# Optimization experiments

Hardware: AMD Instinct MI355X
Metric: run time of the kernel (lower is better)

Reference implementation:

```python
import jax, jax.numpy as jnp
import numpy as np

ALPHA = 0.4
STEPS = 4
EPSILON = 0.005

N_NODES = 4096
N_EDGES = 131072
D_FEAT = 128


def setup_inputs() -> dict:
    key = jax.random.key(0)
    k1, k2, k3, k4 = jax.random.split(key, 4)
    x = jax.random.normal(k1, (N_NODES, D_FEAT), dtype=jnp.float32)
    src = jax.random.randint(k2, (N_EDGES,), 0, N_NODES)
    dst = jax.random.randint(k3, (N_EDGES,), 0, N_NODES)
    edge_index = jnp.stack([src, dst], axis=0).astype(jnp.int64)
    edge_attr = jax.random.uniform(k4, (N_EDGES,), dtype=jnp.float32)
    return {"x": x, "edge_index": edge_index, "edge_attr": edge_attr}


def reference(x, edge_index, edge_attr):
    # PPR power series: result = sum_i theta_i * A_i, where
    #   A_0 = edge pattern with unit values, A_1 = A (edge_attr),
    #   A_{i+1} = threshold_eps(A @ A_i).
    # Dense [N,N] representation: thresholding (dropping entries < eps in the
    # sparse original) is exactly zeroing those entries here; jit-compatible
    # since sparse nnz is data-dependent.
    N = x.shape[0]
    src, dst = edge_index[0], edge_index[1]
    A = jnp.zeros((N, N), dtype=edge_attr.dtype).at[src, dst].add(edge_attr)
    P0 = jnp.zeros((N, N), dtype=edge_attr.dtype).at[src, dst].add(1.0)

    mats = [P0, A]
    for _ in range(1, STEPS - 1):
        M = A @ mats[-1]
        M = jnp.where(M >= EPSILON, M, jnp.zeros((), dtype=M.dtype))
        mats.append(M)

    thetas = [ALPHA * (1.0 - ALPHA) ** i for i in range(STEPS)]
    out = thetas[0] * mats[0]
    for t, m in zip(thetas[1:], mats[1:]):
        out = out + t * m
    return out
```

## Files before the change

kernel.cpp:

```cpp
#include <hip/hip_runtime.h>
#include <hip/hip_fp16.h>

#define N_NODES 4096
#define EPS 0.005f
#define TH0 0.4f
#define TH1 0.24f
#define TH2 0.144f
#define TH3 0.0864f
#define JTILE 512
#define NTILES (N_NODES / JTILE)
#define RCAP 80
#define CPAD 16

typedef float v4f __attribute__((ext_vector_type(4)));
typedef unsigned int u32x4 __attribute__((ext_vector_type(4)));


static __device__ __forceinline__ unsigned short f2h(float f) {
    return __half_as_ushort(__float2half(f));
}

__global__ void scatter_kernel(const int* __restrict__ idx,
                               const float* __restrict__ attr, int E,
                               int* __restrict__ counts, int2* __restrict__ pairs) {
    int e = blockIdx.x * blockDim.x + threadIdx.x;
    if (e < E) {
        int s = idx[e];
        int d = idx[e + E];
        float a = attr[e];
        int pos = atomicAdd(&counts[s * CPAD], 1);
        if (pos < RCAP) pairs[s * RCAP + pos] = make_int2(d, __float_as_int(a));
    }
}

__global__ __launch_bounds__(256)
void m2_kernel(const int* __restrict__ counts, const int2* __restrict__ pairs,
               unsigned short* __restrict__ m2) {
    __shared__ float acc[N_NODES];
    __shared__ int   kcol[RCAP];
    __shared__ float kval[RCAP];
    __shared__ int   kcnt[RCAP];
    int i = blockIdx.x;
    int t = threadIdx.x;
    float4 z = make_float4(0.f, 0.f, 0.f, 0.f);
    for (int j4 = t; j4 < N_NODES / 4; j4 += 256) ((float4*)acc)[j4] = z;
    int cnt = min(counts[i * CPAD], RCAP);
    if (t < cnt) {
        int2 p = pairs[i * RCAP + t];
        kcol[t] = p.x;
        kval[t] = __int_as_float(p.y);
        kcnt[t] = min(counts[p.x * CPAD], RCAP);
    }
    __syncthreads();
    int gid = t >> 3, gl = t & 7;
    int2 zp = make_int2(0, 0);
    for (int q = gid; q < cnt; q += 32) {
        float a = kval[q];
        int fb = kcol[q] * RCAP;
        int fn = kcnt[q];
        for (int f0 = gl; f0 < fn; f0 += 32) {
            int i1 = f0 + 8, i2 = f0 + 16, i3 = f0 + 24;
            int2 p0 = pairs[fb + f0];
            int2 p1 = (i1 < fn) ? pairs[fb + i1] : zp;
            int2 p2 = (i2 < fn) ? pairs[fb + i2] : zp;
            int2 p3 = (i3 < fn) ? pairs[fb + i3] : zp;
            unsafeAtomicAdd(&acc[p0.x], a * __int_as_float(p0.y));
            unsafeAtomicAdd(&acc[p1.x], a * __int_as_float(p1.y));
            unsafeAtomicAdd(&acc[p2.x], a * __int_as_float(p2.y));
            unsafeAtomicAdd(&acc[p3.x], a * __int_as_float(p3.y));
        }
    }
    __syncthreads();
    size_t rb = (size_t)i * N_NODES;
    for (int j4 = t; j4 < N_NODES / 4; j4 += 256) {
        float4 v = ((const float4*)acc)[j4];
        ushort4 r;
        r.x = (v.x >= EPS) ? f2h(v.x) : (unsigned short)0;
        r.y = (v.y >= EPS) ? f2h(v.y) : (unsigned short)0;
        r.z = (v.z >= EPS) ? f2h(v.z) : (unsigned short)0;
        r.w = (v.w >= EPS) ? f2h(v.w) : (unsigned short)0;
        ((ushort4*)(m2 + rb))[j4] = r;
    }
}

#define MIX2(uu_word, aclo, achi, aa)                                          \
    asm("v_fma_mix_f32 %0, %1, %2, %0 op_sel_hi:[0,1,0]"                       \
        : "+v"(aclo) : "v"(aa), "v"(uu_word));                                 \
    asm("v_fma_mix_f32 %0, %1, %2, %0 op_sel:[0,1,0] op_sel_hi:[0,1,0]"        \
        : "+v"(achi) : "v"(aa), "v"(uu_word));

#define MIX8(uu, aa)                                                           \
    MIX2(uu.x, ac0, ac1, aa) MIX2(uu.y, ac2, ac3, aa)                          \
    MIX2(uu.z, ac4, ac5, aa) MIX2(uu.w, ac6, ac7, aa)

__global__ __launch_bounds__(128)
void out_kernel(const int* __restrict__ counts, const int2* __restrict__ pairs,
                const unsigned short* __restrict__ m2,
                float* __restrict__ out) {
    __shared__ float ap[2][JTILE];
    int lin = blockIdx.x;
    int tile = lin & 7;
    int jb = tile * JTILE;
    int t = threadIdx.x;
    int w = t >> 6, lane = t & 63;
    int i = 2 * (lin >> 3) + w;
    float* apw = ap[w];
    ((float4*)apw)[lane] = make_float4(0.f, 0.f, 0.f, 0.f);
    ((float4*)apw)[64 + lane] = make_float4(0.f, 0.f, 0.f, 0.f);
    int cnt = min(counts[i * CPAD], RCAP);
    const int2* pi = pairs + i * RCAP;
    for (int e = lane; e < cnt; e += 64) {
        int2 p = pi[e];
        int cl = p.x - jb;
        if ((unsigned)cl < (unsigned)JTILE)
            unsafeAtomicAdd(&apw[cl], TH0 + TH1 * __int_as_float(p.y));
    }
    int cnt8 = (cnt + 7) & ~7;
    const unsigned short* m2l = m2 + jb + 8 * lane;
    float ac0 = 0.f, ac1 = 0.f, ac2 = 0.f, ac3 = 0.f;
    float ac4 = 0.f, ac5 = 0.f, ac6 = 0.f, ac7 = 0.f;
    for (int e = 0; e < cnt8; e += 8) {
        int4 q01 = *(const int4*)(pi + e);
        int4 q23 = *(const int4*)(pi + e + 2);
        int4 q45 = *(const int4*)(pi + e + 4);
        int4 q67 = *(const int4*)(pi + e + 6);
        int k0 = __builtin_amdgcn_readfirstlane(q01.x);
        int k1 = __builtin_amdgcn_readfirstlane(q01.z);
        int k2 = __builtin_amdgcn_readfirstlane(q23.x);
        int k3 = __builtin_amdgcn_readfirstlane(q23.z);
        int k4 = __builtin_amdgcn_readfirstlane(q45.x);
        int k5 = __builtin_amdgcn_readfirstlane(q45.z);
        int k6 = __builtin_amdgcn_readfirstlane(q67.x);
        int k7 = __builtin_amdgcn_readfirstlane(q67.z);
        float a0 = __int_as_float(q01.y), a1 = __int_as_float(q01.w);
        float a2 = __int_as_float(q23.y), a3 = __int_as_float(q23.w);
        float a4 = __int_as_float(q45.y), a5 = __int_as_float(q45.w);
        float a6 = __int_as_float(q67.y), a7 = __int_as_float(q67.w);
        u32x4 u0 = *(const u32x4*)(m2l + (size_t)k0 * N_NODES);
        u32x4 u1 = *(const u32x4*)(m2l + (size_t)k1 * N_NODES);
        u32x4 u2 = *(const u32x4*)(m2l + (size_t)k2 * N_NODES);
        u32x4 u3 = *(const u32x4*)(m2l + (size_t)k3 * N_NODES);
        u32x4 u4 = *(const u32x4*)(m2l + (size_t)k4 * N_NODES);
        u32x4 u5 = *(const u32x4*)(m2l + (size_t)k5 * N_NODES);
        u32x4 u6 = *(const u32x4*)(m2l + (size_t)k6 * N_NODES);
        u32x4 u7 = *(const u32x4*)(m2l + (size_t)k7 * N_NODES);
        MIX8(u0, a0) MIX8(u1, a1) MIX8(u2, a2) MIX8(u3, a3)
        MIX8(u4, a4) MIX8(u5, a5) MIX8(u6, a6) MIX8(u7, a7)
    }
    u32x4 um = *(const u32x4*)(m2 + (size_t)i * N_NODES + jb + 8 * lane);
    unsigned ux = um.x, uy = um.y, uz = um.z, uw = um.w;
    __half2 hx = *(__half2*)&ux, hy = *(__half2*)&uy;
    __half2 hz = *(__half2*)&uz, hw = *(__half2*)&uw;
    float4 p0 = ((const float4*)apw)[2 * lane];
    float4 p1 = ((const float4*)apw)[2 * lane + 1];
    v4f r0, r1;
    r0.x = p0.x + TH2 * __low2float(hx)  + TH3 * ((ac0 >= EPS) ? ac0 : 0.0f);
    r0.y = p0.y + TH2 * __high2float(hx) + TH3 * ((ac1 >= EPS) ? ac1 : 0.0f);
    r0.z = p0.z + TH2 * __low2float(hy)  + TH3 * ((ac2 >= EPS) ? ac2 : 0.0f);
    r0.w = p0.w + TH2 * __high2float(hy) + TH3 * ((ac3 >= EPS) ? ac3 : 0.0f);
    r1.x = p1.x + TH2 * __low2float(hz)  + TH3 * ((ac4 >= EPS) ? ac4 : 0.0f);
    r1.y = p1.y + TH2 * __high2float(hz) + TH3 * ((ac5 >= EPS) ? ac5 : 0.0f);
    r1.z = p1.z + TH2 * __low2float(hw)  + TH3 * ((ac6 >= EPS) ? ac6 : 0.0f);
    r1.w = p1.w + TH2 * __high2float(hw) + TH3 * ((ac7 >= EPS) ? ac7 : 0.0f);
    float* o = out + (size_t)i * N_NODES + jb + 8 * lane;
    __builtin_nontemporal_store(r0, (v4f*)o);
    __builtin_nontemporal_store(r1, (v4f*)(o + 4));
}

extern "C" void kernel_launch(void* const* d_in, const int* in_sizes, int n_in,
                              void* d_out, int out_size, void* d_ws, size_t ws_size,
                              hipStream_t stream) {
    const int* idx = (const int*)d_in[1];
    const float* attr = (const float*)d_in[2];
    int E = in_sizes[1] / 2;

    char* ws = (char*)d_ws;
    int*  counts = (int*)(ws);
    int2* pairs  = (int2*)(ws + (256 << 10));
    unsigned short* m2 = (unsigned short*)(ws + (4 << 20));
    float* out   = (float*)d_out;

    (void)hipMemsetAsync(ws, 0,
                         (256 << 10) + N_NODES * RCAP * sizeof(int2), stream);
    scatter_kernel<<<(E + 255) / 256, 256, 0, stream>>>(idx, attr, E, counts, pairs);
    m2_kernel<<<N_NODES, 256, 0, stream>>>(counts, pairs, m2);
    out_kernel<<<(N_NODES / 2) * NTILES, 128, 0, stream>>>(counts, pairs, m2, out);
}
```

Measured before the change: 187.2 us.

## Halve out_kernel column tile to 256 and gather 16 rows per iteration

```diff
diff --git a/kernel.cpp b/kernel.cpp
--- a/kernel.cpp
+++ b/kernel.cpp
@@ -7,12 +7,13 @@
 #define TH1 0.24f
 #define TH2 0.144f
 #define TH3 0.0864f
-#define JTILE 512
+#define JTILE 256
 #define NTILES (N_NODES / JTILE)
 #define RCAP 80
 #define CPAD 16
 
 typedef float v4f __attribute__((ext_vector_type(4)));
+typedef unsigned int u32x2 __attribute__((ext_vector_type(2)));
 typedef unsigned int u32x4 __attribute__((ext_vector_type(4)));
 
 
@@ -89,9 +90,14 @@
     asm("v_fma_mix_f32 %0, %1, %2, %0 op_sel:[0,1,0] op_sel_hi:[0,1,0]"        \
         : "+v"(achi) : "v"(aa), "v"(uu_word));
 
-#define MIX8(uu, aa)                                                           \
-    MIX2(uu.x, ac0, ac1, aa) MIX2(uu.y, ac2, ac3, aa)                          \
-    MIX2(uu.z, ac4, ac5, aa) MIX2(uu.w, ac6, ac7, aa)
+#define MIX4(uu, aa)                                                           \
+    MIX2(uu.x, ac0, ac1, aa) MIX2(uu.y, ac2, ac3, aa)
+
+#define EX2(q, klo, alo, khi, ahi)                                             \
+    klo = __builtin_amdgcn_readfirstlane(q.x); alo = __int_as_float(q.y);      \
+    khi = __builtin_amdgcn_readfirstlane(q.z); ahi = __int_as_float(q.w);
+
+#define GATH(k, u)  u = *(const u32x2*)(m2l + (size_t)k * N_NODES);
 
 __global__ __launch_bounds__(128)
 void out_kernel(const int* __restrict__ counts, const int2* __restrict__ pairs,
@@ -99,14 +105,13 @@
                 float* __restrict__ out) {
     __shared__ float ap[2][JTILE];
     int lin = blockIdx.x;
-    int tile = lin & 7;
+    int tile = (lin & 7) | ((lin >> 14) << 3);
     int jb = tile * JTILE;
     int t = threadIdx.x;
     int w = t >> 6, lane = t & 63;
-    int i = 2 * (lin >> 3) + w;
+    int i = 2 * ((lin >> 3) & 2047) + w;
     float* apw = ap[w];
     ((float4*)apw)[lane] = make_float4(0.f, 0.f, 0.f, 0.f);
-    ((float4*)apw)[64 + lane] = make_float4(0.f, 0.f, 0.f, 0.f);
     int cnt = min(counts[i * CPAD], RCAP);
     const int2* pi = pairs + i * RCAP;
     for (int e = lane; e < cnt; e += 64) {
@@ -116,55 +121,57 @@
             unsafeAtomicAdd(&apw[cl], TH0 + TH1 * __int_as_float(p.y));
     }
     int cnt8 = (cnt + 7) & ~7;
-    const unsigned short* m2l = m2 + jb + 8 * lane;
+    const unsigned short* m2l = m2 + jb + 4 * lane;
+    const int4* pi4 = (const int4*)pi;
     float ac0 = 0.f, ac1 = 0.f, ac2 = 0.f, ac3 = 0.f;
-    float ac4 = 0.f, ac5 = 0.f, ac6 = 0.f, ac7 = 0.f;
-    for (int e = 0; e < cnt8; e += 8) {
-        int4 q01 = *(const int4*)(pi + e);
-        int4 q23 = *(const int4*)(pi + e + 2);
-        int4 q45 = *(const int4*)(pi + e + 4);
-        int4 q67 = *(const int4*)(pi + e + 6);
-        int k0 = __builtin_amdgcn_readfirstlane(q01.x);
-        int k1 = __builtin_amdgcn_readfirstlane(q01.z);
-        int k2 = __builtin_amdgcn_readfirstlane(q23.x);
-        int k3 = __builtin_amdgcn_readfirstlane(q23.z);
-        int k4 = __builtin_amdgcn_readfirstlane(q45.x);
-        int k5 = __builtin_amdgcn_readfirstlane(q45.z);
-        int k6 = __builtin_amdgcn_readfirstlane(q67.x);
-        int k7 = __builtin_amdgcn_readfirstlane(q67.z);
-        float a0 = __int_as_float(q01.y), a1 = __int_as_float(q01.w);
-        float a2 = __int_as_float(q23.y), a3 = __int_as_float(q23.w);
-        float a4 = __int_as_float(q45.y), a5 = __int_as_float(q45.w);
-        float a6 = __int_as_float(q67.y), a7 = __int_as_float(q67.w);
-        u32x4 u0 = *(const u32x4*)(m2l + (size_t)k0 * N_NODES);
-        u32x4 u1 = *(const u32x4*)(m2l + (size_t)k1 * N_NODES);
-        u32x4 u2 = *(const u32x4*)(m2l + (size_t)k2 * N_NODES);
-        u32x4 u3 = *(const u32x4*)(m2l + (size_t)k3 * N_NODES);
-        u32x4 u4 = *(const u32x4*)(m2l + (size_t)k4 * N_NODES);
-        u32x4 u5 = *(const u32x4*)(m2l + (size_t)k5 * N_NODES);
-        u32x4 u6 = *(const u32x4*)(m2l + (size_t)k6 * N_NODES);
-        u32x4 u7 = *(const u32x4*)(m2l + (size_t)k7 * N_NODES);
-        MIX8(u0, a0) MIX8(u1, a1) MIX8(u2, a2) MIX8(u3, a3)
-        MIX8(u4, a4) MIX8(u5, a5) MIX8(u6, a6) MIX8(u7, a7)
+
+    int e = 0;
+    for (; e + 16 <= cnt8; e += 16) {
+        int4 q0 = pi4[(e >> 1) + 0], q1 = pi4[(e >> 1) + 1];
+        int4 q2 = pi4[(e >> 1) + 2], q3 = pi4[(e >> 1) + 3];
+        int4 q4 = pi4[(e >> 1) + 4], q5 = pi4[(e >> 1) + 5];
+        int4 q6 = pi4[(e >> 1) + 6], q7 = pi4[(e >> 1) + 7];
+        int k0, k1, k2, k3, k4, k5, k6, k7, k8, k9, kA, kB, kC, kD, kE, kF;
+        float a0, a1, a2, a3, a4, a5, a6, a7, a8, a9, aA, aB, aC, aD, aE, aF;
+        EX2(q0, k0, a0, k1, a1) EX2(q1, k2, a2, k3, a3)
+        EX2(q2, k4, a4, k5, a5) EX2(q3, k6, a6, k7, a7)
+        EX2(q4, k8, a8, k9, a9) EX2(q5, kA, aA, kB, aB)
+        EX2(q6, kC, aC, kD, aD) EX2(q7, kE, aE, kF, aF)
+        u32x2 u0, u1, u2, u3, u4, u5, u6, u7, u8, u9, uA, uB, uC, uD, uE, uF;
+        GATH(k0, u0) GATH(k1, u1) GATH(k2, u2) GATH(k3, u3)
+        GATH(k4, u4) GATH(k5, u5) GATH(k6, u6) GATH(k7, u7)
+        GATH(k8, u8) GATH(k9, u9) GATH(kA, uA) GATH(kB, uB)
+        GATH(kC, uC) GATH(kD, uD) GATH(kE, uE) GATH(kF, uF)
+        MIX4(u0, a0) MIX4(u1, a1) MIX4(u2, a2) MIX4(u3, a3)
+        MIX4(u4, a4) MIX4(u5, a5) MIX4(u6, a6) MIX4(u7, a7)
+        MIX4(u8, a8) MIX4(u9, a9) MIX4(uA, aA) MIX4(uB, aB)
+        MIX4(uC, aC) MIX4(uD, aD) MIX4(uE, aE) MIX4(uF, aF)
     }
-    u32x4 um = *(const u32x4*)(m2 + (size_t)i * N_NODES + jb + 8 * lane);
-    unsigned ux = um.x, uy = um.y, uz = um.z, uw = um.w;
+    if (e < cnt8) {
+        int4 q0 = pi4[(e >> 1) + 0], q1 = pi4[(e >> 1) + 1];
+        int4 q2 = pi4[(e >> 1) + 2], q3 = pi4[(e >> 1) + 3];
+        int k0, k1, k2, k3, k4, k5, k6, k7;
+        float a0, a1, a2, a3, a4, a5, a6, a7;
+        EX2(q0, k0, a0, k1, a1) EX2(q1, k2, a2, k3, a3)
+        EX2(q2, k4, a4, k5, a5) EX2(q3, k6, a6, k7, a7)
+        u32x2 u0, u1, u2, u3, u4, u5, u6, u7;
+        GATH(k0, u0) GATH(k1, u1) GATH(k2, u2) GATH(k3, u3)
+        GATH(k4, u4) GATH(k5, u5) GATH(k6, u6) GATH(k7, u7)
+        MIX4(u0, a0) MIX4(u1, a1) MIX4(u2, a2) MIX4(u3, a3)
+        MIX4(u4, a4) MIX4(u5, a5) MIX4(u6, a6) MIX4(u7, a7)
+    }
+
+    u32x2 um = *(const u32x2*)(m2 + (size_t)i * N_NODES + jb + 4 * lane);
+    unsigned ux = um.x, uy = um.y;
     __half2 hx = *(__half2*)&ux, hy = *(__half2*)&uy;
-    __half2 hz = *(__half2*)&uz, hw = *(__half2*)&uw;
-    float4 p0 = ((const float4*)apw)[2 * lane];
-    float4 p1 = ((const float4*)apw)[2 * lane + 1];
-    v4f r0, r1;
+    float4 p0 = ((const float4*)apw)[lane];
+    v4f r0;
     r0.x = p0.x + TH2 * __low2float(hx)  + TH3 * ((ac0 >= EPS) ? ac0 : 0.0f);
     r0.y = p0.y + TH2 * __high2float(hx) + TH3 * ((ac1 >= EPS) ? ac1 : 0.0f);
     r0.z = p0.z + TH2 * __low2float(hy)  + TH3 * ((ac2 >= EPS) ? ac2 : 0.0f);
     r0.w = p0.w + TH2 * __high2float(hy) + TH3 * ((ac3 >= EPS) ? ac3 : 0.0f);
-    r1.x = p1.x + TH2 * __low2float(hz)  + TH3 * ((ac4 >= EPS) ? ac4 : 0.0f);
-    r1.y = p1.y + TH2 * __high2float(hz) + TH3 * ((ac5 >= EPS) ? ac5 : 0.0f);
-    r1.z = p1.z + TH2 * __low2float(hw)  + TH3 * ((ac6 >= EPS) ? ac6 : 0.0f);
-    r1.w = p1.w + TH2 * __high2float(hw) + TH3 * ((ac7 >= EPS) ? ac7 : 0.0f);
-    float* o = out + (size_t)i * N_NODES + jb + 8 * lane;
+    float* o = out + (size_t)i * N_NODES + jb + 4 * lane;
     __builtin_nontemporal_store(r0, (v4f*)o);
-    __builtin_nontemporal_store(r1, (v4f*)(o + 4));
 }
 
 extern "C" void kernel_launch(void* const* d_in, const int* in_sizes, int n_in,
```

Result: slower. 224.2 us (+19.8%).
